# Kernel tuning notes

Hardware: AMD Instinct MI355X
Metric: run time of the kernel (lower is better)

Reference implementation:

```python
import jax, jax.numpy as jnp
import numpy as np

DIM = 512
HEADS = 8
SEQ = 2048
BATCH = 4


def setup_inputs() -> dict:
    key = jax.random.key(0)
    k = jax.random.split(key, 6)
    x = jax.random.normal(k[0], (BATCH, SEQ, DIM), dtype=jnp.float32)
    mask = jax.random.normal(k[1], (BATCH, SEQ, SEQ), dtype=jnp.float32)
    Wqkv = jax.random.normal(k[2], (3 * DIM, DIM), dtype=jnp.float32) * 0.02
    Btab = jax.random.normal(k[3], (1, HEADS, 2 * SEQ - 1), dtype=jnp.float32) * 0.02
    Wproj = jax.random.normal(k[4], (DIM, DIM), dtype=jnp.float32) * 0.02
    bproj = jax.random.normal(k[5], (DIM,), dtype=jnp.float32) * 0.02
    return {"x": x, "mask": mask, "Wqkv": Wqkv, "Btab": Btab,
            "Wproj": Wproj, "bproj": bproj}


def reference(x, mask, Wqkv, Btab, Wproj, bproj):
    B, N, C = x.shape
    H = Btab.shape[1]
    seq = (Btab.shape[2] + 1) // 2
    head_dim = C // H
    scale = head_dim ** (-0.5)

    # qkv projection (no bias), split into q,k,v of shape [B,H,N,head_dim]
    qkv = (x @ Wqkv.T).reshape(B, N, 3, H, head_dim)
    qkv = jnp.transpose(qkv, (2, 0, 3, 1, 4))  # [3,B,H,N,hd]
    q, k, v = qkv[0], qkv[1], qkv[2]

    # gathered relative-position bias: B_index[i,j] = i - j + seq - 1
    idx = jnp.arange(N)[:, None] - jnp.arange(N)[None, :] + (seq - 1)  # [N,N]
    bias = Btab[:, :, idx]  # [1,H,N,N]

    attn = jnp.einsum('bhnd,bhmd->bhnm', q, k) * scale + bias
    attn = attn + mask[:, None, :, :]  # additive mask, broadcast over heads
    attn = jax.nn.softmax(attn, axis=-1)

    out = jnp.einsum('bhnm,bhmd->bhnd', attn, v)  # [B,H,N,hd]
    out = jnp.transpose(out, (0, 2, 1, 3)).reshape(B, N, C)
    return out @ Wproj.T + bproj
```

## Files before the change

kernel.cpp:

```cpp
#include <hip/hip_runtime.h>


typedef __attribute__((ext_vector_type(8))) short short8;
typedef __attribute__((ext_vector_type(4))) float f32x4;

#define SEQ   2048
#define NHEAD 8
#define NBATCH 4
#define HD    64
#define CDIM  512

__device__ __forceinline__ unsigned short f32_to_bf16_rn(float f) {
  unsigned u = __builtin_bit_cast(unsigned, f);
  u += 0x7FFFu + ((u >> 16) & 1u);
  return (unsigned short)(u >> 16);
}

__global__ __launch_bounds__(256) void cvt_f32_bf16(const float* __restrict__ in,
                                                    ushort* __restrict__ out, int n4) {
  int i = blockIdx.x * 256 + threadIdx.x;
  const int stride = gridDim.x * 256;
  for (; i < n4; i += stride) {
    float4 v = reinterpret_cast<const float4*>(in)[i];
    ushort4 o;
    o.x = f32_to_bf16_rn(v.x);
    o.y = f32_to_bf16_rn(v.y);
    o.z = f32_to_bf16_rn(v.z);
    o.w = f32_to_bf16_rn(v.w);
    reinterpret_cast<ushort4*>(out)[i] = o;
  }
}

template <int MODE>
__global__ __launch_bounds__(256) void gemm_nt(
    const ushort* __restrict__ A, const ushort* __restrict__ Bm,
    ushort* __restrict__ qo, ushort* __restrict__ ko, ushort* __restrict__ vto,
    const float* __restrict__ bias, float* __restrict__ outf) {
  const int K = 512;
  __shared__ ushort As[128 * 40];
  __shared__ ushort Bs[128 * 40];

  const int t = threadIdx.x;
  const int bn = blockIdx.x, bm = blockIdx.y;
  const int lane = t & 63, w = t >> 6;
  const int wm = w >> 1, wn = w & 1;
  const int lr = lane & 15, lq = lane >> 4;
  const int m0 = bm * 128, n0 = bn * 128;

  f32x4 acc[4][4];
#pragma unroll
  for (int i = 0; i < 4; ++i)
#pragma unroll
    for (int j = 0; j < 4; ++j) acc[i][j] = (f32x4){0.f, 0.f, 0.f, 0.f};

  for (int kt = 0; kt < K; kt += 32) {
#pragma unroll
    for (int p = 0; p < 2; ++p) {
      const int flat = p * 256 + t;
      const int row = flat >> 2, seg = flat & 3;
      *(uint4*)&As[row * 40 + seg * 8] =
          *(const uint4*)(A + (size_t)(m0 + row) * K + kt + seg * 8);
      *(uint4*)&Bs[row * 40 + seg * 8] =
          *(const uint4*)(Bm + (size_t)(n0 + row) * K + kt + seg * 8);
    }
    __syncthreads();

    short8 af[4], bf[4];
#pragma unroll
    for (int i = 0; i < 4; ++i) {
      af[i] = *(const short8*)&As[(wm * 64 + i * 16 + lr) * 40 + lq * 8];
      bf[i] = *(const short8*)&Bs[(wn * 64 + i * 16 + lr) * 40 + lq * 8];
    }
#pragma unroll
    for (int i = 0; i < 4; ++i)
#pragma unroll
      for (int j = 0; j < 4; ++j)
        acc[i][j] = __builtin_amdgcn_mfma_f32_16x16x32_bf16(af[i], bf[j], acc[i][j], 0, 0, 0);
    __syncthreads();
  }

  if constexpr (MODE == 0) {
#pragma unroll
    for (int i = 0; i < 4; ++i) {
      const int mbase = m0 + wm * 64 + i * 16 + lq * 4;
      const int bb = mbase >> 11;
      const int s0 = mbase & 2047;
#pragma unroll
      for (int j = 0; j < 4; ++j) {
        const int nb = n0 + wn * 64 + j * 16;
        const int tt = nb >> 9;
        const int hh = (nb >> 6) & 7;
        const int d0 = nb & 63;
        const int bh = bb * NHEAD + hh;
        if (tt == 2) {
          ushort4 pk;
          pk.x = f32_to_bf16_rn(acc[i][j][0]);
          pk.y = f32_to_bf16_rn(acc[i][j][1]);
          pk.z = f32_to_bf16_rn(acc[i][j][2]);
          pk.w = f32_to_bf16_rn(acc[i][j][3]);
          *(ushort4*)(vto + ((size_t)bh * HD + d0 + lr) * SEQ + s0) = pk;
        } else {
          ushort* dst = (tt == 0) ? qo : ko;
#pragma unroll
          for (int r = 0; r < 4; ++r)
            dst[((size_t)bh * SEQ + s0 + r) * HD + d0 + lr] = f32_to_bf16_rn(acc[i][j][r]);
        }
      }
    }
  } else {
#pragma unroll
    for (int i = 0; i < 4; ++i) {
#pragma unroll
      for (int j = 0; j < 4; ++j) {
        const int n = n0 + wn * 64 + j * 16 + lr;
        const float bv = bias[n];
#pragma unroll
        for (int r = 0; r < 4; ++r) {
          const int m = m0 + wm * 64 + i * 16 + lq * 4 + r;
          outf[(size_t)m * 512 + n] = acc[i][j][r] + bv;
        }
      }
    }
  }
}

__global__ __launch_bounds__(256) void attn_fused(
    const ushort* __restrict__ Q, const ushort* __restrict__ Kt,
    const ushort* __restrict__ VT, const float* __restrict__ mask,
    const float* __restrict__ Btab, ushort* __restrict__ Out) {
  __shared__ ushort Ks[2][64 * 72];
  __shared__ ushort Vs[2][64 * 72];
  __shared__ ushort Ps[4][32 * 68];
  __shared__ ushort Bw[2176];

  const int flat = blockIdx.x;
  const int xcd = flat & 7;
  const int rr = flat >> 3;
  const int h = rr & 7;
  const int slot = rr >> 3;
  const int g = slot * 8 + xcd;
  const int qt = g & 15, b = g >> 4;

  const int bh = b * NHEAD + h;
  const ushort* qh = Q + (size_t)bh * SEQ * HD;
  const ushort* kh = Kt + (size_t)bh * SEQ * HD;
  const ushort* vh = VT + (size_t)bh * HD * SEQ;
  const float* mb = mask + (size_t)b * SEQ * SEQ;
  const float* bt = Btab + h * (2 * SEQ - 1);

  const int t = threadIdx.x;
  const int lane = t & 63, w = t >> 6;
  const int lr = lane & 15, lq = lane >> 4;
  const int qb0 = qt * 128;
  const int qbaseA = qb0 + w * 32;
  const int qbaseB = qbaseA + 16;

  for (int i = t; i < 2175; i += 256)
    Bw[i] = f32_to_bf16_rn(bt[qb0 + i] * 1.44269504f);

  short8 qfA0, qfA1, qfB0, qfB1;
  {
    const ushort* qpA = qh + (size_t)(qbaseA + lr) * HD + lq * 8;
    qfA0 = *(const short8*)qpA;
    qfA1 = *(const short8*)(qpA + 32);
    const ushort* qpB = qh + (size_t)(qbaseB + lr) * HD + lq * 8;
    qfB0 = *(const short8*)qpB;
    qfB1 = *(const short8*)(qpB + 32);
  }

  const float* mrowA[4];
  const float* mrowB[4];
#pragma unroll
  for (int r = 0; r < 4; ++r) {
    mrowA[r] = mb + (size_t)(qbaseA + lq * 4 + r) * SEQ + lr;
    mrowB[r] = mb + (size_t)(qbaseB + lq * 4 + r) * SEQ + lr;
  }

  float lA0 = 0.f, lA1 = 0.f, lA2 = 0.f, lA3 = 0.f;
  float lB0 = 0.f, lB1 = 0.f, lB2 = 0.f, lB3 = 0.f;
  f32x4 ofA[4], ofB[4];
#pragma unroll
  for (int i = 0; i < 4; ++i) {
    ofA[i] = (f32x4){0.f, 0.f, 0.f, 0.f};
    ofB[i] = (f32x4){0.f, 0.f, 0.f, 0.f};
  }

  const int qrlA = w * 32 + lq * 4;
  const int srow = t >> 3;
  const int sseg = t & 7;

  const ushort* kp = kh + (size_t)srow * HD + sseg * 8;
  const ushort* vp = vh + (size_t)srow * SEQ + sseg * 8;

  uint4 kr0 = *(const uint4*)(kp);
  uint4 kr1 = *(const uint4*)(kp + 32 * HD);
  uint4 vr0 = *(const uint4*)(vp);
  uint4 vr1 = *(const uint4*)(vp + 32 * SEQ);
  *(uint4*)&Ks[0][srow * 72 + sseg * 8] = kr0;
  *(uint4*)&Ks[0][(32 + srow) * 72 + sseg * 8] = kr1;
  *(uint4*)&Vs[0][srow * 72 + sseg * 8] = vr0;
  *(uint4*)&Vs[0][(32 + srow) * 72 + sseg * 8] = vr1;
  kr0 = *(const uint4*)(kp + 64 * HD);
  kr1 = *(const uint4*)(kp + 96 * HD);
  vr0 = *(const uint4*)(vp + 64);
  vr1 = *(const uint4*)(vp + 64 + 32 * SEQ);

  float mnA[4][4];
#pragma unroll
  for (int f = 0; f < 4; ++f)
#pragma unroll
    for (int r = 0; r < 4; ++r) mnA[f][r] = mrowA[r][f * 16];

  for (int it = 0; it < 32; ++it) {
    const int kv0 = it * 64;
    const int cur = it & 1, nxt = cur ^ 1;

    __syncthreads();

    *(uint4*)&Ks[nxt][srow * 72 + sseg * 8] = kr0;
    *(uint4*)&Ks[nxt][(32 + srow) * 72 + sseg * 8] = kr1;
    *(uint4*)&Vs[nxt][srow * 72 + sseg * 8] = vr0;
    *(uint4*)&Vs[nxt][(32 + srow) * 72 + sseg * 8] = vr1;

    float mnB[4][4];
#pragma unroll
    for (int f = 0; f < 4; ++f)
#pragma unroll
      for (int r = 0; r < 4; ++r) mnB[f][r] = mrowB[r][kv0 + f * 16];

    const int lkv = (it + 2 < 32) ? (it + 2) * 64 : 0;
    kr0 = *(const uint4*)(kp + (size_t)lkv * HD);
    kr1 = *(const uint4*)(kp + (size_t)(lkv + 32) * HD);
    vr0 = *(const uint4*)(vp + lkv);
    vr1 = *(const uint4*)(vp + lkv + 32 * SEQ);

    f32x4 sfA[4], sfB[4];
#pragma unroll
    for (int f = 0; f < 4; ++f) {
      const ushort* kfp = &Ks[cur][(f * 16 + lr) * 72 + lq * 8];
      const short8 k0 = *(const short8*)kfp;
      const short8 k1 = *(const short8*)(kfp + 32);
      sfA[f] = (f32x4){0.f, 0.f, 0.f, 0.f};
      sfA[f] = __builtin_amdgcn_mfma_f32_16x16x32_bf16(qfA0, k0, sfA[f], 0, 0, 0);
      sfA[f] = __builtin_amdgcn_mfma_f32_16x16x32_bf16(qfA1, k1, sfA[f], 0, 0, 0);
      sfB[f] = (f32x4){0.f, 0.f, 0.f, 0.f};
      sfB[f] = __builtin_amdgcn_mfma_f32_16x16x32_bf16(qfB0, k0, sfB[f], 0, 0, 0);
      sfB[f] = __builtin_amdgcn_mfma_f32_16x16x32_bf16(qfB1, k1, sfB[f], 0, 0, 0);
    }

#pragma unroll
    for (int f = 0; f < 4; ++f) {
      const int ib = qrlA - (kv0 + f * 16 + lr) + 2047;
#pragma unroll
      for (int r = 0; r < 4; ++r) {
        const float bw = __builtin_bit_cast(float, ((unsigned)Bw[ib + r]) << 16);
        const float xs = fmaf(sfA[f][r], 0.18033688f,
                              fmaf(mnA[f][r], 1.44269504f, bw));
        const float p = __builtin_amdgcn_exp2f(xs);
        if (r == 0) lA0 += p; else if (r == 1) lA1 += p;
        else if (r == 2) lA2 += p; else lA3 += p;
        const unsigned u = __builtin_bit_cast(unsigned, p);
        Ps[w][(lq * 4 + r) * 68 + f * 16 + lr] =
            (unsigned short)((u + 0x8000u) >> 16);
      }
    }

    const int mkv = (it + 1 < 32) ? (it + 1) * 64 : 0;
#pragma unroll
    for (int f = 0; f < 4; ++f)
#pragma unroll
      for (int r = 0; r < 4; ++r) mnA[f][r] = mrowA[r][mkv + f * 16];

#pragma unroll
    for (int f = 0; f < 4; ++f) {
      const int ib = qrlA + 16 - (kv0 + f * 16 + lr) + 2047;
#pragma unroll
      for (int r = 0; r < 4; ++r) {
        const float bw = __builtin_bit_cast(float, ((unsigned)Bw[ib + r]) << 16);
        const float xs = fmaf(sfB[f][r], 0.18033688f,
                              fmaf(mnB[f][r], 1.44269504f, bw));
        const float p = __builtin_amdgcn_exp2f(xs);
        if (r == 0) lB0 += p; else if (r == 1) lB1 += p;
        else if (r == 2) lB2 += p; else lB3 += p;
        const unsigned u = __builtin_bit_cast(unsigned, p);
        Ps[w][(16 + lq * 4 + r) * 68 + f * 16 + lr] =
            (unsigned short)((u + 0x8000u) >> 16);
      }
    }

#pragma unroll
    for (int ks = 0; ks < 2; ++ks) {
      union { uint2 u[2]; short8 s; } puA, puB;
      const int pbase = ks * 32 + lq * 8;
      puA.u[0] = *(const uint2*)&Ps[w][lr * 68 + pbase];
      puA.u[1] = *(const uint2*)&Ps[w][lr * 68 + pbase + 4];
      puB.u[0] = *(const uint2*)&Ps[w][(16 + lr) * 68 + pbase];
      puB.u[1] = *(const uint2*)&Ps[w][(16 + lr) * 68 + pbase + 4];
#pragma unroll
      for (int hf = 0; hf < 4; ++hf) {
        const short8 vf =
            *(const short8*)&Vs[cur][(hf * 16 + lr) * 72 + ks * 32 + lq * 8];
        ofA[hf] = __builtin_amdgcn_mfma_f32_16x16x32_bf16(puA.s, vf, ofA[hf], 0, 0, 0);
        ofB[hf] = __builtin_amdgcn_mfma_f32_16x16x32_bf16(puB.s, vf, ofB[hf], 0, 0, 0);
      }
    }
  }

  float lA[4] = {lA0, lA1, lA2, lA3};
  float lB[4] = {lB0, lB1, lB2, lB3};
#pragma unroll
  for (int r = 0; r < 4; ++r) {
    float v = lA[r];
    v += __shfl_xor(v, 1); v += __shfl_xor(v, 2);
    v += __shfl_xor(v, 4); v += __shfl_xor(v, 8);
    lA[r] = v;
    float u = lB[r];
    u += __shfl_xor(u, 1); u += __shfl_xor(u, 2);
    u += __shfl_xor(u, 4); u += __shfl_xor(u, 8);
    lB[r] = u;
  }
#pragma unroll
  for (int r = 0; r < 4; ++r) {
    const float invA = 1.0f / lA[r];
    const int qrA = qbaseA + lq * 4 + r;
    ushort* opA = Out + ((size_t)(b * SEQ + qrA)) * CDIM + h * HD;
#pragma unroll
    for (int hf = 0; hf < 4; ++hf) opA[hf * 16 + lr] = f32_to_bf16_rn(ofA[hf][r] * invA);
    const float invB = 1.0f / lB[r];
    const int qrB = qbaseB + lq * 4 + r;
    ushort* opB = Out + ((size_t)(b * SEQ + qrB)) * CDIM + h * HD;
#pragma unroll
    for (int hf = 0; hf < 4; ++hf) opB[hf * 16 + lr] = f32_to_bf16_rn(ofB[hf][r] * invB);
  }
}

extern "C" void kernel_launch(void* const* d_in, const int* in_sizes, int n_in,
                              void* d_out, int out_size, void* d_ws, size_t ws_size,
                              hipStream_t stream) {
  const float* x     = (const float*)d_in[0];
  const float* mask  = (const float*)d_in[1];
  const float* Wqkv  = (const float*)d_in[2];
  const float* Btab  = (const float*)d_in[3];
  const float* Wproj = (const float*)d_in[4];
  const float* bproj = (const float*)d_in[5];
  float* out = (float*)d_out;

  char* ws = (char*)d_ws;
  const size_t SZ_X   = (size_t)NBATCH * SEQ * CDIM;
  const size_t SZ_QKV = (size_t)3 * CDIM * CDIM;
  const size_t SZ_PRJ = (size_t)CDIM * CDIM;
  const size_t SZ_HD  = (size_t)NBATCH * NHEAD * SEQ * HD;

  ushort* xb    = (ushort*)ws; ws += SZ_X * 2;
  ushort* wqkvb = (ushort*)ws; ws += SZ_QKV * 2;
  ushort* wprjb = (ushort*)ws; ws += SZ_PRJ * 2;
  ushort* qb    = (ushort*)ws; ws += SZ_HD * 2;
  ushort* kb    = (ushort*)ws; ws += SZ_HD * 2;
  ushort* vtb   = (ushort*)ws; ws += SZ_HD * 2;
  ushort* aob   = (ushort*)ws; ws += SZ_X * 2;

  {
    int n4 = (int)(SZ_X / 4);
    int g = (n4 + 255) / 256; if (g > 4096) g = 4096;
    cvt_f32_bf16<<<g, 256, 0, stream>>>(x, xb, n4);
  }
  {
    int n4 = (int)(SZ_QKV / 4);
    cvt_f32_bf16<<<(n4 + 255) / 256, 256, 0, stream>>>(Wqkv, wqkvb, n4);
  }
  {
    int n4 = (int)(SZ_PRJ / 4);
    cvt_f32_bf16<<<(n4 + 255) / 256, 256, 0, stream>>>(Wproj, wprjb, n4);
  }

  gemm_nt<0><<<dim3(12, 64), 256, 0, stream>>>(xb, wqkvb, qb, kb, vtb, nullptr, nullptr);

  attn_fused<<<dim3(512), 256, 0, stream>>>(qb, kb, vtb, mask, Btab, aob);

  gemm_nt<1><<<dim3(4, 64), 256, 0, stream>>>(aob, wprjb, nullptr, nullptr, nullptr, bproj, out);
}
```

Measured before the change: 146.4 us.

## Transpose QK^T MFMA output so mask loads are float4 and P stores packed

Swaps the MFMA operand order so each lane holds four consecutive key columns of one query row instead of four query rows. The mask is then read with float4 loads rather than scalar strided loads, and P is written to shared memory as packed uint2 with a 72-element row stride, read back as uint4. Row sums now reduce across lane groups with two shuffles plus a broadcast shuffle at the end. The intent is to cut global mask load instructions and LDS store traffic in the softmax loop, at the cost of reworked bias indexing.

```diff
diff --git a/kernel.cpp b/kernel.cpp
--- a/kernel.cpp
+++ b/kernel.cpp
@@ -9,6 +9,7 @@
 #define NBATCH 4
 #define HD    64
 #define CDIM  512
+#define L2E   1.44269504f
 
 __device__ __forceinline__ unsigned short f32_to_bf16_rn(float f) {
   unsigned u = __builtin_bit_cast(unsigned, f);
@@ -130,7 +131,7 @@
     const float* __restrict__ Btab, ushort* __restrict__ Out) {
   __shared__ ushort Ks[2][64 * 72];
   __shared__ ushort Vs[2][64 * 72];
-  __shared__ ushort Ps[4][32 * 68];
+  __shared__ ushort Ps[4][32 * 72];
   __shared__ ushort Bw[2176];
 
   const int flat = blockIdx.x;
@@ -156,7 +157,7 @@
   const int qbaseB = qbaseA + 16;
 
   for (int i = t; i < 2175; i += 256)
-    Bw[i] = f32_to_bf16_rn(bt[qb0 + i] * 1.44269504f);
+    Bw[i] = f32_to_bf16_rn(bt[qb0 + i] * L2E);
 
   short8 qfA0, qfA1, qfB0, qfB1;
   {
@@ -168,16 +169,12 @@
     qfB1 = *(const short8*)(qpB + 32);
   }
 
-  const float* mrowA[4];
-  const float* mrowB[4];
-#pragma unroll
-  for (int r = 0; r < 4; ++r) {
-    mrowA[r] = mb + (size_t)(qbaseA + lq * 4 + r) * SEQ + lr;
-    mrowB[r] = mb + (size_t)(qbaseB + lq * 4 + r) * SEQ + lr;
-  }
-
-  float lA0 = 0.f, lA1 = 0.f, lA2 = 0.f, lA3 = 0.f;
-  float lB0 = 0.f, lB1 = 0.f, lB2 = 0.f, lB3 = 0.f;
+  const float* mvA = mb + (size_t)(qbaseA + lr) * SEQ + 4 * lq;
+  const float* mvB = mb + (size_t)(qbaseB + lr) * SEQ + 4 * lq;
+  const int bwA0 = w * 32 + lr - 4 * lq + 2047;
+  const int bwB0 = bwA0 + 16;
+
+  float lAa = 0.f, lAb = 0.f, lBa = 0.f, lBb = 0.f;
   f32x4 ofA[4], ofB[4];
 #pragma unroll
   for (int i = 0; i < 4; ++i) {
@@ -185,7 +182,6 @@
     ofB[i] = (f32x4){0.f, 0.f, 0.f, 0.f};
   }
 
-  const int qrlA = w * 32 + lq * 4;
   const int srow = t >> 3;
   const int sseg = t & 7;
 
@@ -205,11 +201,9 @@
   vr0 = *(const uint4*)(vp + 64);
   vr1 = *(const uint4*)(vp + 64 + 32 * SEQ);
 
-  float mnA[4][4];
-#pragma unroll
-  for (int f = 0; f < 4; ++f)
-#pragma unroll
-    for (int r = 0; r < 4; ++r) mnA[f][r] = mrowA[r][f * 16];
+  float4 mnA[4];
+#pragma unroll
+  for (int f = 0; f < 4; ++f) mnA[f] = *(const float4*)(mvA + f * 16);
 
   for (int it = 0; it < 32; ++it) {
     const int kv0 = it * 64;
@@ -222,11 +216,10 @@
     *(uint4*)&Vs[nxt][srow * 72 + sseg * 8] = vr0;
     *(uint4*)&Vs[nxt][(32 + srow) * 72 + sseg * 8] = vr1;
 
-    float mnB[4][4];
+    float4 mnB[4];
 #pragma unroll
     for (int f = 0; f < 4; ++f)
-#pragma unroll
-      for (int r = 0; r < 4; ++r) mnB[f][r] = mrowB[r][kv0 + f * 16];
+      mnB[f] = *(const float4*)(mvB + kv0 + f * 16);
 
     const int lkv = (it + 2 < 32) ? (it + 2) * 64 : 0;
     kr0 = *(const uint4*)(kp + (size_t)lkv * HD);
@@ -241,61 +234,67 @@
       const short8 k0 = *(const short8*)kfp;
       const short8 k1 = *(const short8*)(kfp + 32);
       sfA[f] = (f32x4){0.f, 0.f, 0.f, 0.f};
-      sfA[f] = __builtin_amdgcn_mfma_f32_16x16x32_bf16(qfA0, k0, sfA[f], 0, 0, 0);
-      sfA[f] = __builtin_amdgcn_mfma_f32_16x16x32_bf16(qfA1, k1, sfA[f], 0, 0, 0);
+      sfA[f] = __builtin_amdgcn_mfma_f32_16x16x32_bf16(k0, qfA0, sfA[f], 0, 0, 0);
+      sfA[f] = __builtin_amdgcn_mfma_f32_16x16x32_bf16(k1, qfA1, sfA[f], 0, 0, 0);
       sfB[f] = (f32x4){0.f, 0.f, 0.f, 0.f};
-      sfB[f] = __builtin_amdgcn_mfma_f32_16x16x32_bf16(qfB0, k0, sfB[f], 0, 0, 0);
-      sfB[f] = __builtin_amdgcn_mfma_f32_16x16x32_bf16(qfB1, k1, sfB[f], 0, 0, 0);
+      sfB[f] = __builtin_amdgcn_mfma_f32_16x16x32_bf16(k0, qfB0, sfB[f], 0, 0, 0);
+      sfB[f] = __builtin_amdgcn_mfma_f32_16x16x32_bf16(k1, qfB1, sfB[f], 0, 0, 0);
     }
 
 #pragma unroll
     for (int f = 0; f < 4; ++f) {
-      const int ib = qrlA - (kv0 + f * 16 + lr) + 2047;
+      const int ibA = bwA0 - kv0 - 16 * f;
+      unsigned up0, up1;
 #pragma unroll
       for (int r = 0; r < 4; ++r) {
-        const float bw = __builtin_bit_cast(float, ((unsigned)Bw[ib + r]) << 16);
+        const float bwv =
+            __builtin_bit_cast(float, ((unsigned)Bw[ibA - r]) << 16);
         const float xs = fmaf(sfA[f][r], 0.18033688f,
-                              fmaf(mnA[f][r], 1.44269504f, bw));
+                              fmaf((&mnA[f].x)[r], L2E, bwv));
         const float p = __builtin_amdgcn_exp2f(xs);
-        if (r == 0) lA0 += p; else if (r == 1) lA1 += p;
-        else if (r == 2) lA2 += p; else lA3 += p;
-        const unsigned u = __builtin_bit_cast(unsigned, p);
-        Ps[w][(lq * 4 + r) * 68 + f * 16 + lr] =
-            (unsigned short)((u + 0x8000u) >> 16);
-      }
+        if (f & 1) lAb += p; else lAa += p;
+        const unsigned hh = (__builtin_bit_cast(unsigned, p) + 0x8000u) >> 16;
+        if (r == 0) up0 = hh;
+        else if (r == 1) up0 |= hh << 16;
+        else if (r == 2) up1 = hh;
+        else up1 |= hh << 16;
+      }
+      uint2 pk; pk.x = up0; pk.y = up1;
+      *(uint2*)&Ps[w][lr * 72 + 16 * f + 4 * lq] = pk;
     }
 
     const int mkv = (it + 1 < 32) ? (it + 1) * 64 : 0;
 #pragma unroll
     for (int f = 0; f < 4; ++f)
-#pragma unroll
-      for (int r = 0; r < 4; ++r) mnA[f][r] = mrowA[r][mkv + f * 16];
+      mnA[f] = *(const float4*)(mvA + mkv + f * 16);
 
 #pragma unroll
     for (int f = 0; f < 4; ++f) {
-      const int ib = qrlA + 16 - (kv0 + f * 16 + lr) + 2047;
+      const int ibB = bwB0 - kv0 - 16 * f;
+      unsigned up0, up1;
 #pragma unroll
       for (int r = 0; r < 4; ++r) {
-        const float bw = __builtin_bit_cast(float, ((unsigned)Bw[ib + r]) << 16);
+        const float bwv =
+            __builtin_bit_cast(float, ((unsigned)Bw[ibB - r]) << 16);
         const float xs = fmaf(sfB[f][r], 0.18033688f,
-                              fmaf(mnB[f][r], 1.44269504f, bw));
+                              fmaf((&mnB[f].x)[r], L2E, bwv));
         const float p = __builtin_amdgcn_exp2f(xs);
-        if (r == 0) lB0 += p; else if (r == 1) lB1 += p;
-        else if (r == 2) lB2 += p; else lB3 += p;
-        const unsigned u = __builtin_bit_cast(unsigned, p);
-        Ps[w][(16 + lq * 4 + r) * 68 + f * 16 + lr] =
-            (unsigned short)((u + 0x8000u) >> 16);
-      }
+        if (f & 1) lBb += p; else lBa += p;
+        const unsigned hh = (__builtin_bit_cast(unsigned, p) + 0x8000u) >> 16;
+        if (r == 0) up0 = hh;
+        else if (r == 1) up0 |= hh << 16;
+        else if (r == 2) up1 = hh;
+        else up1 |= hh << 16;
+      }
+      uint2 pk; pk.x = up0; pk.y = up1;
+      *(uint2*)&Ps[w][(16 + lr) * 72 + 16 * f + 4 * lq] = pk;
     }
 
 #pragma unroll
     for (int ks = 0; ks < 2; ++ks) {
-      union { uint2 u[2]; short8 s; } puA, puB;
-      const int pbase = ks * 32 + lq * 8;
-      puA.u[0] = *(const uint2*)&Ps[w][lr * 68 + pbase];
-      puA.u[1] = *(const uint2*)&Ps[w][lr * 68 + pbase + 4];
-      puB.u[0] = *(const uint2*)&Ps[w][(16 + lr) * 68 + pbase];
-      puB.u[1] = *(const uint2*)&Ps[w][(16 + lr) * 68 + pbase + 4];
+      union { uint4 u; short8 s; } puA, puB;
+      puA.u = *(const uint4*)&Ps[w][lr * 72 + ks * 32 + lq * 8];
+      puB.u = *(const uint4*)&Ps[w][(16 + lr) * 72 + ks * 32 + lq * 8];
 #pragma unroll
       for (int hf = 0; hf < 4; ++hf) {
         const short8 vf =
@@ -306,27 +305,19 @@
     }
   }
 
-  float lA[4] = {lA0, lA1, lA2, lA3};
-  float lB[4] = {lB0, lB1, lB2, lB3};
+  float vA = lAa + lAb;
+  vA += __shfl_xor(vA, 16); vA += __shfl_xor(vA, 32);
+  float vB = lBa + lBb;
+  vB += __shfl_xor(vB, 16); vB += __shfl_xor(vB, 32);
+
 #pragma unroll
   for (int r = 0; r < 4; ++r) {
-    float v = lA[r];
-    v += __shfl_xor(v, 1); v += __shfl_xor(v, 2);
-    v += __shfl_xor(v, 4); v += __shfl_xor(v, 8);
-    lA[r] = v;
-    float u = lB[r];
-    u += __shfl_xor(u, 1); u += __shfl_xor(u, 2);
-    u += __shfl_xor(u, 4); u += __shfl_xor(u, 8);
-    lB[r] = u;
-  }
-#pragma unroll
-  for (int r = 0; r < 4; ++r) {
-    const float invA = 1.0f / lA[r];
+    const float invA = 1.0f / __shfl(vA, (lane & 48) | (lq * 4 + r));
     const int qrA = qbaseA + lq * 4 + r;
     ushort* opA = Out + ((size_t)(b * SEQ + qrA)) * CDIM + h * HD;
 #pragma unroll
     for (int hf = 0; hf < 4; ++hf) opA[hf * 16 + lr] = f32_to_bf16_rn(ofA[hf][r] * invA);
-    const float invB = 1.0f / lB[r];
+    const float invB = 1.0f / __shfl(vB, (lane & 48) | (lq * 4 + r));
     const int qrB = qbaseB + lq * 4 + r;
     ushort* opB = Out + ((size_t)(b * SEQ + qrB)) * CDIM + h * HD;
 #pragma unroll
```

Result: slower. 157.1 us (+7.3%).
